# Performance work log

Measured on AMD Instinct MI355X. Metric: run time of the kernel, lower is better.

## Reference

```python
import jax, jax.numpy as jnp
import numpy as np

N_SENT, N_DOC, G = 100000, 10000, 32

def _seg_mean_right(x, src, dst, n_dst):
    # DGL GraphConv(norm='right'): sum incoming messages / in_degree (clamped to 1)
    m = jax.ops.segment_sum(x[src], dst, num_segments=n_dst)
    deg = jax.ops.segment_sum(jnp.ones_like(dst, dtype=x.dtype), dst, num_segments=n_dst)
    return m / jnp.maximum(deg, 1.0)[:, None]

def _rel_layer(xs, xd, coeff, basis, loop_w, bias,
               src_ss, dst_ss, src_sd, dst_sd, src_ds, dst_ds):
    # WeightBasis: per-relation weight = sum_b coeff[r,b] * basis[b]
    W = jnp.einsum('rb,bio->rio', coeff, basis)  # [3, in, out]
    # rel 0: sent->doc, rel 1: doc->sent, rel 2: sent->sent; HeteroGraphConv sums per dst ntype
    h_doc = _seg_mean_right(xs, src_sd, dst_sd, N_DOC) @ W[0]
    h_sent = (_seg_mean_right(xd, src_ds, dst_ds, N_SENT) @ W[1]
              + _seg_mean_right(xs, src_ss, dst_ss, N_SENT) @ W[2])
    h_sent = jax.nn.relu(h_sent + xs @ loop_w + bias)
    h_doc = jax.nn.relu(h_doc + xd @ loop_w + bias)
    return h_sent, h_doc

def setup_inputs() -> dict:
    key = jax.random.key(0)
    ks = jax.random.split(key, 20)
    d_in, d_h, d_o = 768, 256, 128
    inp = {
        'x_sent': jax.random.normal(ks[0], (N_SENT, d_in), jnp.float32),
        'x_doc': jax.random.normal(ks[1], (N_DOC, d_in), jnp.float32),
        'coeff1': jax.random.normal(ks[2], (3, 2), jnp.float32),
        'basis1': jax.random.normal(ks[3], (2, d_in, d_h), jnp.float32) * 0.02,
        'loop_w1': jax.random.normal(ks[4], (d_in, d_h), jnp.float32) * 0.02,
        'bias1': jnp.zeros((d_h,), jnp.float32),
        'coeff2': jax.random.normal(ks[5], (3, 2), jnp.float32),
        'basis2': jax.random.normal(ks[6], (2, d_h, d_o), jnp.float32) * 0.05,
        'loop_w2': jax.random.normal(ks[7], (d_h, d_o), jnp.float32) * 0.05,
        'bias2': jnp.zeros((d_o,), jnp.float32),
        'w_score': jax.random.normal(ks[8], (d_o, 1), jnp.float32) * 0.05,
        'b_score': jnp.zeros((1,), jnp.float32),
        'src_ss': jax.random.randint(ks[9], (400000,), 0, N_SENT, jnp.int32),
        'dst_ss': jax.random.randint(ks[10], (400000,), 0, N_SENT, jnp.int32),
        'src_sd': jax.random.randint(ks[11], (100000,), 0, N_SENT, jnp.int32),
        'dst_sd': jax.random.randint(ks[12], (100000,), 0, N_DOC, jnp.int32),
        'src_ds': jax.random.randint(ks[13], (100000,), 0, N_DOC, jnp.int32),
        'dst_ds': jax.random.randint(ks[14], (100000,), 0, N_SENT, jnp.int32),
        'gid_sent': jnp.sort(jax.random.randint(ks[15], (N_SENT,), 0, G, jnp.int32)),
        'gid_doc': jnp.sort(jax.random.randint(ks[16], (N_DOC,), 0, G, jnp.int32)),
        'num_graphs': G,
    }
    return inp

def reference(x_sent, x_doc, coeff1, basis1, loop_w1, bias1,
              coeff2, basis2, loop_w2, bias2, w_score, b_score,
              src_ss, dst_ss, src_sd, dst_sd, src_ds, dst_ds,
              gid_sent, gid_doc, num_graphs):
    h_s, h_d = _rel_layer(x_sent, x_doc, coeff1, basis1, loop_w1, bias1,
                          src_ss, dst_ss, src_sd, dst_sd, src_ds, dst_ds)
    h_s, h_d = _rel_layer(h_s, h_d, coeff2, basis2, loop_w2, bias2,
                          src_ss, dst_ss, src_sd, dst_sd, src_ds, dst_ds)
    # dgl.sum_nodes over batched graph, summed across ntypes
    readout = (jax.ops.segment_sum(h_s, gid_sent, num_segments=num_graphs)
               + jax.ops.segment_sum(h_d, gid_doc, num_segments=num_graphs))
    return readout @ w_score + b_score  # [G, 1]
```

## Files before the change

kernel.cpp:

```cpp
#include <hip/hip_runtime.h>

#define CDIV(a,b) (((a)+(b)-1)/(b))

typedef __attribute__((ext_vector_type(8))) short bf16x8;
typedef __attribute__((ext_vector_type(4))) float floatx4;

__device__ __forceinline__ ushort f2bf(float x) {
    unsigned u = __float_as_uint(x);
    return (ushort)((u + 0x7fffu + ((u >> 16) & 1u)) >> 16);
}
__device__ __forceinline__ float bflo(unsigned v) { return __uint_as_float(v << 16); }
__device__ __forceinline__ float bfhi(unsigned v) { return __uint_as_float(v & 0xffff0000u); }

__device__ __forceinline__ void load_lds16(const ushort* g, ushort* l) {
    __builtin_amdgcn_global_load_lds(
        (const __attribute__((address_space(1))) void*)g,
        (__attribute__((address_space(3))) void*)l, 16, 0, 0);
}


__global__ void zero_f4(float4* __restrict__ p, long long n4) {
    long long i = blockIdx.x * 256LL + threadIdx.x;
    if (i < n4) p[i] = make_float4(0.f, 0.f, 0.f, 0.f);
}

__global__ void cvt_bf16_k(const float4* __restrict__ in, uint4* __restrict__ out, long long n8) {
    long long i = blockIdx.x * 256LL + threadIdx.x;
    if (i >= n8) return;
    float4 a = in[2 * i], b = in[2 * i + 1];
    uint4 o;
    o.x = (unsigned)f2bf(a.x) | ((unsigned)f2bf(a.y) << 16);
    o.y = (unsigned)f2bf(a.z) | ((unsigned)f2bf(a.w) << 16);
    o.z = (unsigned)f2bf(b.x) | ((unsigned)f2bf(b.y) << 16);
    o.w = (unsigned)f2bf(b.z) | ((unsigned)f2bf(b.w) << 16);
    out[i] = o;
}

__global__ void fill_basis_T(ushort* __restrict__ out, int K, int col0,
                             const float* __restrict__ basis, long long KN,
                             const float* __restrict__ coeff, int r, int N, long long total) {
    long long i = blockIdx.x * 256LL + threadIdx.x;
    if (i >= total) return;
    int k = (int)(i % K), n = (int)(i / K);
    float c0 = coeff[2 * r], c1 = coeff[2 * r + 1];
    out[(size_t)(col0 + n) * K + k] = f2bf(c0 * basis[(size_t)k * N + n] + c1 * basis[KN + (size_t)k * N + n]);
}

__global__ void fill_copy_T(ushort* __restrict__ out, int K, int col0,
                            const float* __restrict__ src, int N, long long total) {
    long long i = blockIdx.x * 256LL + threadIdx.x;
    if (i >= total) return;
    int k = (int)(i % K), n = (int)(i / K);
    out[(size_t)(col0 + n) * K + k] = f2bf(src[(size_t)k * N + n]);
}


__global__ void accum_deg_i(const int* __restrict__ dst, int n, int slot, int* __restrict__ deg) {
    int i = blockIdx.x * 256 + threadIdx.x;
    if (i < n) atomicAdd(&deg[slot + dst[i]], 1);
}

__global__ void scan_p1(const int* __restrict__ deg, int n, int* __restrict__ bsum) {
    __shared__ int sd[256];
    int blk = blockIdx.x, tid = threadIdx.x;
    int i0 = blk * 1024 + tid * 4;
    int s = 0;
#pragma unroll
    for (int j = 0; j < 4; ++j) if (i0 + j < n) s += deg[i0 + j];
    sd[tid] = s; __syncthreads();
    for (int o = 128; o; o >>= 1) {
        if (tid < o) sd[tid] += sd[tid + o];
        __syncthreads();
    }
    if (tid == 0) bsum[blk] = sd[0];
}

__global__ void scan_p2(int* __restrict__ bsum, int nb, int* __restrict__ rowptr, int ntot, int etot) {
    __shared__ int sd[256];
    int tid = threadIdx.x;
    int v = (tid < nb) ? bsum[tid] : 0;
    sd[tid] = v; __syncthreads();
    for (int o = 1; o < 256; o <<= 1) {
        int t = (tid >= o) ? sd[tid - o] : 0;
        __syncthreads();
        sd[tid] += t;
        __syncthreads();
    }
    if (tid < nb) bsum[tid] = sd[tid] - v;
    if (tid == 0) rowptr[ntot] = etot;
}

__global__ void scan_p3(const int* __restrict__ deg, int n, const int* __restrict__ bsum,
                        int* __restrict__ rowptr) {
    __shared__ int sd[256];
    int blk = blockIdx.x, tid = threadIdx.x;
    int i0 = blk * 1024 + tid * 4;
    int v[4]; int s = 0;
#pragma unroll
    for (int j = 0; j < 4; ++j) { v[j] = (i0 + j < n) ? deg[i0 + j] : 0; s += v[j]; }
    sd[tid] = s; __syncthreads();
    for (int o = 1; o < 256; o <<= 1) {
        int t = (tid >= o) ? sd[tid - o] : 0;
        __syncthreads();
        sd[tid] += t;
        __syncthreads();
    }
    int excl = bsum[blk] + sd[tid] - s;
#pragma unroll
    for (int j = 0; j < 4; ++j) {
        if (i0 + j < n) rowptr[i0 + j] = excl;
        excl += v[j];
    }
}

__global__ void fill_csr(const int* __restrict__ src, const int* __restrict__ dst, int n, int slot,
                         const int* __restrict__ rowptr, int* __restrict__ fill, int* __restrict__ col) {
    int i = blockIdx.x * 256 + threadIdx.x;
    if (i >= n) return;
    int d = slot + dst[i];
    int p = rowptr[d] + atomicAdd(&fill[d], 1);
    col[p] = src[i];
}

__global__ __launch_bounds__(256) void gemm_bf16(
    const ushort* __restrict__ A, const ushort* __restrict__ Bt, ushort* __restrict__ C,
    int M, int K, int N) {
    __shared__ ushort As[128 * 32];
    __shared__ ushort Bs[128 * 32];
    const int tid = threadIdx.x;
    const int bn = blockIdx.x * 128;
    const long long bm = blockIdx.y * 128LL;
    const int lane = tid & 63, wave = tid >> 6;
    const int mo = (wave & 1) * 64, no = (wave >> 1) * 64;
    const int l15 = lane & 15, quad = lane >> 4;
    const int srow0 = wave * 16 + (lane >> 2);
    const int schunk = (lane & 3) * 8;
    floatx4 acc[4][4] = {};

    for (int k0 = 0; k0 < K; k0 += 32) {
#pragma unroll
        for (int t = 0; t < 2; ++t) {
            int row = t * 64 + srow0;
            long long ar = bm + row; if (ar >= M) ar = M - 1;
            load_lds16(A + ar * (size_t)K + k0 + schunk, As + t * 2048 + wave * 512);
            load_lds16(Bt + (size_t)(bn + row) * K + k0 + schunk, Bs + t * 2048 + wave * 512);
        }
        __syncthreads();
        bf16x8 af[4], bfr[4];
#pragma unroll
        for (int mt = 0; mt < 4; ++mt)
            af[mt] = *(const bf16x8*)(As + (mo + mt * 16 + l15) * 32 + quad * 8);
#pragma unroll
        for (int nt = 0; nt < 4; ++nt)
            bfr[nt] = *(const bf16x8*)(Bs + (no + nt * 16 + l15) * 32 + quad * 8);
#pragma unroll
        for (int mt = 0; mt < 4; ++mt)
#pragma unroll
            for (int nt = 0; nt < 4; ++nt)
                acc[mt][nt] = __builtin_amdgcn_mfma_f32_16x16x32_bf16(af[mt], bfr[nt], acc[mt][nt], 0, 0, 0);
        __syncthreads();
    }
#pragma unroll
    for (int mt = 0; mt < 4; ++mt)
#pragma unroll
        for (int i = 0; i < 4; ++i) {
            long long row = bm + mo + mt * 16 + quad * 4 + i;
            if (row < M) {
#pragma unroll
                for (int nt = 0; nt < 4; ++nt)
                    C[row * (size_t)N + bn + no + nt * 16 + l15] = f2bf(acc[mt][nt][i]);
            }
        }
}


__global__ __launch_bounds__(256) void fused_sent_l1(
    const ushort* __restrict__ ys, const ushort* __restrict__ yd,
    const int* __restrict__ rowptr, const int* __restrict__ col,
    const float* __restrict__ bias, ushort* __restrict__ hout, int NS) {
    int d = blockIdx.x * 4 + (threadIdx.x >> 6);
    if (d >= NS) return;
    int lane = threadIdx.x & 63;
    int cb = lane * 4;
    float a0 = 0, a1 = 0, a2 = 0, a3 = 0;
    int s0 = rowptr[d], s1 = rowptr[d + 1];
    for (int e = s0; e < s1; ++e) {
        int s = col[e];
        uint2 v = *(const uint2*)(ys + (size_t)s * 768 + 256 + cb);
        a0 += bflo(v.x); a1 += bfhi(v.x); a2 += bflo(v.y); a3 += bfhi(v.y);
    }
    float inv = 1.f / (float)max(s1 - s0, 1);
    float m0 = a0 * inv, m1 = a1 * inv, m2 = a2 * inv, m3 = a3 * inv;
    a0 = a1 = a2 = a3 = 0.f;
    int t0 = rowptr[NS + d], t1 = rowptr[NS + d + 1];
    for (int e = t0; e < t1; ++e) {
        int s = col[e];
        uint2 v = *(const uint2*)(yd + (size_t)s * 512 + cb);
        a0 += bflo(v.x); a1 += bfhi(v.x); a2 += bflo(v.y); a3 += bfhi(v.y);
    }
    inv = 1.f / (float)max(t1 - t0, 1);
    uint2 lv = *(const uint2*)(ys + (size_t)d * 768 + 512 + cb);
    float h0 = fmaxf(m0 + a0 * inv + bflo(lv.x) + bias[cb + 0], 0.f);
    float h1 = fmaxf(m1 + a1 * inv + bfhi(lv.x) + bias[cb + 1], 0.f);
    float h2 = fmaxf(m2 + a2 * inv + bflo(lv.y) + bias[cb + 2], 0.f);
    float h3 = fmaxf(m3 + a3 * inv + bfhi(lv.y) + bias[cb + 3], 0.f);
    uint2 o;
    o.x = (unsigned)f2bf(h0) | ((unsigned)f2bf(h1) << 16);
    o.y = (unsigned)f2bf(h2) | ((unsigned)f2bf(h3) << 16);
    *(uint2*)(hout + (size_t)d * 256 + cb) = o;
}

__global__ __launch_bounds__(256) void fused_doc_l1(
    const ushort* __restrict__ ys, const ushort* __restrict__ yd,
    const int* __restrict__ rowptr, const int* __restrict__ col,
    const float* __restrict__ bias, ushort* __restrict__ hout, int NS, int ND) {
    int d = blockIdx.x * 4 + (threadIdx.x >> 6);
    if (d >= ND) return;
    int lane = threadIdx.x & 63;
    int cb = lane * 4;
    float a0 = 0, a1 = 0, a2 = 0, a3 = 0;
    int s0 = rowptr[2 * NS + d], s1 = rowptr[2 * NS + d + 1];
    for (int e = s0; e < s1; ++e) {
        int s = col[e];
        uint2 v = *(const uint2*)(ys + (size_t)s * 768 + cb);
        a0 += bflo(v.x); a1 += bfhi(v.x); a2 += bflo(v.y); a3 += bfhi(v.y);
    }
    float inv = 1.f / (float)max(s1 - s0, 1);
    uint2 lv = *(const uint2*)(yd + (size_t)d * 512 + 256 + cb);
    float h0 = fmaxf(a0 * inv + bflo(lv.x) + bias[cb + 0], 0.f);
    float h1 = fmaxf(a1 * inv + bfhi(lv.x) + bias[cb + 1], 0.f);
    float h2 = fmaxf(a2 * inv + bflo(lv.y) + bias[cb + 2], 0.f);
    float h3 = fmaxf(a3 * inv + bfhi(lv.y) + bias[cb + 3], 0.f);
    uint2 o;
    o.x = (unsigned)f2bf(h0) | ((unsigned)f2bf(h1) << 16);
    o.y = (unsigned)f2bf(h2) | ((unsigned)f2bf(h3) << 16);
    *(uint2*)(hout + (size_t)d * 256 + cb) = o;
}

__global__ __launch_bounds__(256) void fused_sent_l2(
    const ushort* __restrict__ ys, const ushort* __restrict__ yd,
    const int* __restrict__ rowptr, const int* __restrict__ col,
    const float* __restrict__ bias, const float* __restrict__ w,
    const int* __restrict__ gid, float* __restrict__ out, int NS, int G) {
    __shared__ float part[4][32];
    const int tid = threadIdx.x;
    const int lane = tid & 63, wv = tid >> 6;
    const int cb = lane * 2;
    float racc = 0.f;
    const int nw = gridDim.x * 4;
    for (int d = blockIdx.x * 4 + wv; d < NS; d += nw) {
        float a0 = 0.f, a1 = 0.f;
        int s0 = rowptr[d], s1 = rowptr[d + 1];
        for (int e = s0; e < s1; ++e) {
            int s = col[e];
            unsigned v = *(const unsigned*)(ys + (size_t)s * 384 + 128 + cb);
            a0 += bflo(v); a1 += bfhi(v);
        }
        float inv = 1.f / (float)max(s1 - s0, 1);
        float m0 = a0 * inv, m1 = a1 * inv;
        a0 = 0.f; a1 = 0.f;
        int t0 = rowptr[NS + d], t1 = rowptr[NS + d + 1];
        for (int e = t0; e < t1; ++e) {
            int s = col[e];
            unsigned v = *(const unsigned*)(yd + (size_t)s * 256 + cb);
            a0 += bflo(v); a1 += bfhi(v);
        }
        inv = 1.f / (float)max(t1 - t0, 1);
        unsigned lv = *(const unsigned*)(ys + (size_t)d * 384 + 256 + cb);
        float h0 = fmaxf(m0 + a0 * inv + bflo(lv) + bias[cb + 0], 0.f);
        float h1 = fmaxf(m1 + a1 * inv + bfhi(lv) + bias[cb + 1], 0.f);
        float sc = h0 * w[cb] + h1 * w[cb + 1];
#pragma unroll
        for (int o = 32; o; o >>= 1) sc += __shfl_down(sc, o);
        sc = __shfl(sc, 0);
        if (lane == gid[d]) racc += sc;
    }
    if (lane < 32) part[wv][lane] = racc;
    __syncthreads();
    if (tid < G) atomicAdd(&out[tid], part[0][tid] + part[1][tid] + part[2][tid] + part[3][tid]);
}

__global__ __launch_bounds__(256) void fused_doc_l2(
    const ushort* __restrict__ ys, const ushort* __restrict__ yd,
    const int* __restrict__ rowptr, const int* __restrict__ col,
    const float* __restrict__ bias, const float* __restrict__ w,
    const int* __restrict__ gid, float* __restrict__ out, int NS, int ND, int G) {
    __shared__ float part[4][32];
    const int tid = threadIdx.x;
    const int lane = tid & 63, wv = tid >> 6;
    const int cb = lane * 2;
    float racc = 0.f;
    const int nw = gridDim.x * 4;
    for (int d = blockIdx.x * 4 + wv; d < ND; d += nw) {
        float a0 = 0.f, a1 = 0.f;
        int s0 = rowptr[2 * NS + d], s1 = rowptr[2 * NS + d + 1];
        for (int e = s0; e < s1; ++e) {
            int s = col[e];
            unsigned v = *(const unsigned*)(ys + (size_t)s * 384 + cb);
            a0 += bflo(v); a1 += bfhi(v);
        }
        float inv = 1.f / (float)max(s1 - s0, 1);
        unsigned lv = *(const unsigned*)(yd + (size_t)d * 256 + 128 + cb);
        float h0 = fmaxf(a0 * inv + bflo(lv) + bias[cb + 0], 0.f);
        float h1 = fmaxf(a1 * inv + bfhi(lv) + bias[cb + 1], 0.f);
        float sc = h0 * w[cb] + h1 * w[cb + 1];
#pragma unroll
        for (int o = 32; o; o >>= 1) sc += __shfl_down(sc, o);
        sc = __shfl(sc, 0);
        if (lane == gid[d]) racc += sc;
    }
    if (lane < 32) part[wv][lane] = racc;
    __syncthreads();
    if (tid < G) atomicAdd(&out[tid], part[0][tid] + part[1][tid] + part[2][tid] + part[3][tid]);
}

__global__ void init_out(float* __restrict__ out, const float* __restrict__ b, int G) {
    int i = threadIdx.x;
    if (i < G) out[i] = b[0];
}


extern "C" void kernel_launch(void* const* d_in, const int* in_sizes, int n_in,
                              void* d_out, int out_size, void* d_ws, size_t ws_size,
                              hipStream_t stream) {
    const float* x_sent = (const float*)d_in[0];
    const float* x_doc  = (const float*)d_in[1];
    const float* coeff1 = (const float*)d_in[2];
    const float* basis1 = (const float*)d_in[3];
    const float* loopw1 = (const float*)d_in[4];
    const float* bias1  = (const float*)d_in[5];
    const float* coeff2 = (const float*)d_in[6];
    const float* basis2 = (const float*)d_in[7];
    const float* loopw2 = (const float*)d_in[8];
    const float* bias2  = (const float*)d_in[9];
    const float* wscore = (const float*)d_in[10];
    const float* bscore = (const float*)d_in[11];
    const int* src_ss = (const int*)d_in[12];
    const int* dst_ss = (const int*)d_in[13];
    const int* src_sd = (const int*)d_in[14];
    const int* dst_sd = (const int*)d_in[15];
    const int* src_ds = (const int*)d_in[16];
    const int* dst_ds = (const int*)d_in[17];
    const int* gid_sent = (const int*)d_in[18];
    const int* gid_doc  = (const int*)d_in[19];

    const int DIN = 768, DH = 256, DOo = 128;
    const int NS = in_sizes[0] / DIN;
    const int ND = in_sizes[1] / DIN;
    const int E_SS = in_sizes[12], E_SD = in_sizes[14], E_DS = in_sizes[16];
    const int NTOT = NS + NS + ND;
    const int ETOT = E_SS + E_DS + E_SD;
    const int G = out_size;
    float* out = (float*)d_out;

    char* base = (char*)d_ws;
    size_t off = 0;
    auto alloc = [&](size_t bytes) -> char* {
        char* p = base + off;
        off = (off + bytes + 255) & ~(size_t)255;
        return p;
    };
    ushort* B1sT = (ushort*)alloc((size_t)768 * 768 * 2);
    ushort* B1dT = (ushort*)alloc((size_t)512 * 768 * 2);
    ushort* B2sT = (ushort*)alloc((size_t)384 * 256 * 2);
    ushort* B2dT = (ushort*)alloc((size_t)256 * 256 * 2);
    ushort* xs_bf = (ushort*)alloc((size_t)NS * 768 * 2);
    ushort* xd_bf = (ushort*)alloc((size_t)ND * 768 * 2);
    ushort* ys1 = (ushort*)alloc((size_t)NS * 768 * 2);
    ushort* yd1 = (ushort*)alloc((size_t)ND * 512 * 2);
    ushort* h1s = (ushort*)alloc((size_t)NS * 256 * 2);
    ushort* h1d = (ushort*)alloc((size_t)ND * 256 * 2);
    int* deg  = (int*)alloc((size_t)2 * NTOT * 4);
    int* fill = deg + NTOT;
    int* rowptr = (int*)alloc((size_t)(NTOT + 1) * 4);
    int* bsum = (int*)alloc(256 * 4);
    int* colall = (int*)alloc((size_t)ETOT * 4);
    ushort* ys2 = xs_bf;
    ushort* yd2 = xs_bf + (size_t)NS * 384;

    long long t1 = (long long)768 * DH, t2 = (long long)256 * DOo;
    long long KN1 = t1, KN2 = t2;
    int bt1 = (int)CDIV(t1, 256), bt2 = (int)CDIV(t2, 256);
    fill_basis_T<<<bt1, 256, 0, stream>>>(B1sT, 768, 0,       basis1, KN1, coeff1, 0, DH, t1);
    fill_basis_T<<<bt1, 256, 0, stream>>>(B1sT, 768, DH,      basis1, KN1, coeff1, 2, DH, t1);
    fill_copy_T <<<bt1, 256, 0, stream>>>(B1sT, 768, 2 * DH,  loopw1, DH, t1);
    fill_basis_T<<<bt1, 256, 0, stream>>>(B1dT, 768, 0,       basis1, KN1, coeff1, 1, DH, t1);
    fill_copy_T <<<bt1, 256, 0, stream>>>(B1dT, 768, DH,      loopw1, DH, t1);
    fill_basis_T<<<bt2, 256, 0, stream>>>(B2sT, 256, 0,        basis2, KN2, coeff2, 0, DOo, t2);
    fill_basis_T<<<bt2, 256, 0, stream>>>(B2sT, 256, DOo,      basis2, KN2, coeff2, 2, DOo, t2);
    fill_copy_T <<<bt2, 256, 0, stream>>>(B2sT, 256, 2 * DOo,  loopw2, DOo, t2);
    fill_basis_T<<<bt2, 256, 0, stream>>>(B2dT, 256, 0,        basis2, KN2, coeff2, 1, DOo, t2);
    fill_copy_T <<<bt2, 256, 0, stream>>>(B2dT, 256, DOo,      loopw2, DOo, t2);

    cvt_bf16_k<<<(int)CDIV((long long)NS * 768 / 8, 256), 256, 0, stream>>>(
        (const float4*)x_sent, (uint4*)xs_bf, (long long)NS * 768 / 8);
    cvt_bf16_k<<<(int)CDIV((long long)ND * 768 / 8, 256), 256, 0, stream>>>(
        (const float4*)x_doc, (uint4*)xd_bf, (long long)ND * 768 / 8);

    zero_f4<<<(int)CDIV(2 * NTOT / 4, 256), 256, 0, stream>>>((float4*)deg, 2 * NTOT / 4);
    accum_deg_i<<<CDIV(E_SS, 256), 256, 0, stream>>>(dst_ss, E_SS, 0,      deg);
    accum_deg_i<<<CDIV(E_DS, 256), 256, 0, stream>>>(dst_ds, E_DS, NS,     deg);
    accum_deg_i<<<CDIV(E_SD, 256), 256, 0, stream>>>(dst_sd, E_SD, 2 * NS, deg);
    int nb = CDIV(NTOT, 1024);
    scan_p1<<<nb, 256, 0, stream>>>(deg, NTOT, bsum);
    scan_p2<<<1, 256, 0, stream>>>(bsum, nb, rowptr, NTOT, ETOT);
    scan_p3<<<nb, 256, 0, stream>>>(deg, NTOT, bsum, rowptr);
    fill_csr<<<CDIV(E_SS, 256), 256, 0, stream>>>(src_ss, dst_ss, E_SS, 0,      rowptr, fill, colall);
    fill_csr<<<CDIV(E_DS, 256), 256, 0, stream>>>(src_ds, dst_ds, E_DS, NS,     rowptr, fill, colall);
    fill_csr<<<CDIV(E_SD, 256), 256, 0, stream>>>(src_sd, dst_sd, E_SD, 2 * NS, rowptr, fill, colall);

    {
        dim3 g(768 / 128, CDIV(NS, 128));
        gemm_bf16<<<g, 256, 0, stream>>>(xs_bf, B1sT, ys1, NS, 768, 768);
    }
    {
        dim3 g(512 / 128, CDIV(ND, 128));
        gemm_bf16<<<g, 256, 0, stream>>>(xd_bf, B1dT, yd1, ND, 768, 512);
    }
    fused_sent_l1<<<CDIV(NS, 4), 256, 0, stream>>>(ys1, yd1, rowptr, colall, bias1, h1s, NS);
    fused_doc_l1 <<<CDIV(ND, 4), 256, 0, stream>>>(ys1, yd1, rowptr, colall, bias1, h1d, NS, ND);

    {
        dim3 g(384 / 128, CDIV(NS, 128));
        gemm_bf16<<<g, 256, 0, stream>>>(h1s, B2sT, ys2, NS, 256, 384);
    }
    {
        dim3 g(256 / 128, CDIV(ND, 128));
        gemm_bf16<<<g, 256, 0, stream>>>(h1d, B2dT, yd2, ND, 256, 256);
    }
    init_out<<<1, 64, 0, stream>>>(out, bscore, G);
    fused_sent_l2<<<1024, 256, 0, stream>>>(ys2, yd2, rowptr, colall, bias2, wscore, gid_sent, out, NS, G);
    fused_doc_l2 <<<256, 256, 0, stream>>>(ys2, yd2, rowptr, colall, bias2, wscore, gid_doc, out, NS, ND, G);
}
```

Before: 1.169 ms.

## Merge per-relation launches into combined kernels and unroll gather loops

Merges the weight-fill, bf16-conversion, degree-count, CSR-fill and gather kernels into single launches that cover all relations and node types through index-range dispatch. The gather loops are unrolled by four so several neighbor-row loads are in flight at once, and bias and score weights are hoisted into registers. The first sentence GEMM is split into two launches over halves of the rows. These changes cut launch count and raise memory-level parallelism in the gathers, at the cost of more branching inside each kernel.

```diff
diff --git a/kernel.cpp b/kernel.cpp
--- a/kernel.cpp
+++ b/kernel.cpp
@@ -24,40 +24,50 @@
     if (i < n4) p[i] = make_float4(0.f, 0.f, 0.f, 0.f);
 }
 
-__global__ void cvt_bf16_k(const float4* __restrict__ in, uint4* __restrict__ out, long long n8) {
+__global__ void cvt_all(const float4* __restrict__ xs, const float4* __restrict__ xd,
+                        uint4* __restrict__ os, uint4* __restrict__ od,
+                        long long n8s, long long n8d) {
     long long i = blockIdx.x * 256LL + threadIdx.x;
-    if (i >= n8) return;
-    float4 a = in[2 * i], b = in[2 * i + 1];
+    const float4* in; uint4* out; long long j;
+    if (i < n8s) { in = xs; out = os; j = i; }
+    else if (i < n8s + n8d) { in = xd; out = od; j = i - n8s; }
+    else return;
+    float4 a = in[2 * j], b = in[2 * j + 1];
     uint4 o;
     o.x = (unsigned)f2bf(a.x) | ((unsigned)f2bf(a.y) << 16);
     o.y = (unsigned)f2bf(a.z) | ((unsigned)f2bf(a.w) << 16);
     o.z = (unsigned)f2bf(b.x) | ((unsigned)f2bf(b.y) << 16);
     o.w = (unsigned)f2bf(b.z) | ((unsigned)f2bf(b.w) << 16);
-    out[i] = o;
-}
-
-__global__ void fill_basis_T(ushort* __restrict__ out, int K, int col0,
-                             const float* __restrict__ basis, long long KN,
-                             const float* __restrict__ coeff, int r, int N, long long total) {
+    out[j] = o;
+}
+
+__global__ void fill_w5(ushort* __restrict__ BsT, ushort* __restrict__ BdT,
+                        const float* __restrict__ basis, const float* __restrict__ loopw,
+                        const float* __restrict__ coeff, int K, int N, long long KN) {
     long long i = blockIdx.x * 256LL + threadIdx.x;
-    if (i >= total) return;
+    if (i >= KN) return;
     int k = (int)(i % K), n = (int)(i / K);
-    float c0 = coeff[2 * r], c1 = coeff[2 * r + 1];
-    out[(size_t)(col0 + n) * K + k] = f2bf(c0 * basis[(size_t)k * N + n] + c1 * basis[KN + (size_t)k * N + n]);
-}
-
-__global__ void fill_copy_T(ushort* __restrict__ out, int K, int col0,
-                            const float* __restrict__ src, int N, long long total) {
-    long long i = blockIdx.x * 256LL + threadIdx.x;
-    if (i >= total) return;
-    int k = (int)(i % K), n = (int)(i / K);
-    out[(size_t)(col0 + n) * K + k] = f2bf(src[(size_t)k * N + n]);
-}
-
-
-__global__ void accum_deg_i(const int* __restrict__ dst, int n, int slot, int* __restrict__ deg) {
+    int sec = blockIdx.y;
+    float val;
+    if (sec == 2 || sec == 4) {
+        val = loopw[(size_t)k * N + n];
+    } else {
+        int r = (sec == 0) ? 0 : (sec == 1) ? 2 : 1;
+        val = coeff[2 * r] * basis[(size_t)k * N + n] + coeff[2 * r + 1] * basis[KN + (size_t)k * N + n];
+    }
+    ushort* dst = (sec < 3) ? BsT : BdT;
+    int col0 = (sec == 0) ? 0 : (sec == 1) ? N : (sec == 2) ? 2 * N : (sec == 3) ? 0 : N;
+    dst[(size_t)(col0 + n) * K + k] = f2bf(val);
+}
+
+
+__global__ void accum_deg_all(const int* __restrict__ dss, const int* __restrict__ dds,
+                              const int* __restrict__ dsd, int nss, int nds, int nsd,
+                              int NS, int* __restrict__ deg) {
     int i = blockIdx.x * 256 + threadIdx.x;
-    if (i < n) atomicAdd(&deg[slot + dst[i]], 1);
+    if (i < nss) atomicAdd(&deg[dss[i]], 1);
+    else if (i < nss + nds) atomicAdd(&deg[NS + dds[i - nss]], 1);
+    else if (i < nss + nds + nsd) atomicAdd(&deg[2 * NS + dsd[i - nss - nds]], 1);
 }
 
 __global__ void scan_p1(const int* __restrict__ deg, int n, int* __restrict__ bsum) {
@@ -113,13 +123,20 @@
     }
 }
 
-__global__ void fill_csr(const int* __restrict__ src, const int* __restrict__ dst, int n, int slot,
-                         const int* __restrict__ rowptr, int* __restrict__ fill, int* __restrict__ col) {
+__global__ void fill_csr_all(const int* __restrict__ sss, const int* __restrict__ dss,
+                             const int* __restrict__ sds, const int* __restrict__ dds,
+                             const int* __restrict__ ssd, const int* __restrict__ dsd,
+                             int nss, int nds, int nsd, int NS,
+                             const int* __restrict__ rowptr, int* __restrict__ fill,
+                             int* __restrict__ col) {
     int i = blockIdx.x * 256 + threadIdx.x;
-    if (i >= n) return;
-    int d = slot + dst[i];
+    int d, s;
+    if (i < nss) { d = dss[i]; s = sss[i]; }
+    else if (i < nss + nds) { int j = i - nss; d = NS + dds[j]; s = sds[j]; }
+    else if (i < nss + nds + nsd) { int j = i - nss - nds; d = 2 * NS + dsd[j]; s = ssd[j]; }
+    else return;
     int p = rowptr[d] + atomicAdd(&fill[d], 1);
-    col[p] = src[i];
+    col[p] = s;
 }
 
 __global__ __launch_bounds__(256) void gemm_bf16(
@@ -174,140 +191,166 @@
 }
 
 
-__global__ __launch_bounds__(256) void fused_sent_l1(
+__global__ __launch_bounds__(256) void gather_l1(
     const ushort* __restrict__ ys, const ushort* __restrict__ yd,
     const int* __restrict__ rowptr, const int* __restrict__ col,
-    const float* __restrict__ bias, ushort* __restrict__ hout, int NS) {
+    const float* __restrict__ bias, ushort* __restrict__ h1s, ushort* __restrict__ h1d,
+    int NS, int ND) {
     int d = blockIdx.x * 4 + (threadIdx.x >> 6);
-    if (d >= NS) return;
     int lane = threadIdx.x & 63;
     int cb = lane * 4;
-    float a0 = 0, a1 = 0, a2 = 0, a3 = 0;
-    int s0 = rowptr[d], s1 = rowptr[d + 1];
-    for (int e = s0; e < s1; ++e) {
-        int s = col[e];
-        uint2 v = *(const uint2*)(ys + (size_t)s * 768 + 256 + cb);
-        a0 += bflo(v.x); a1 += bfhi(v.x); a2 += bflo(v.y); a3 += bfhi(v.y);
-    }
-    float inv = 1.f / (float)max(s1 - s0, 1);
-    float m0 = a0 * inv, m1 = a1 * inv, m2 = a2 * inv, m3 = a3 * inv;
-    a0 = a1 = a2 = a3 = 0.f;
-    int t0 = rowptr[NS + d], t1 = rowptr[NS + d + 1];
-    for (int e = t0; e < t1; ++e) {
-        int s = col[e];
-        uint2 v = *(const uint2*)(yd + (size_t)s * 512 + cb);
-        a0 += bflo(v.x); a1 += bfhi(v.x); a2 += bflo(v.y); a3 += bfhi(v.y);
-    }
-    inv = 1.f / (float)max(t1 - t0, 1);
-    uint2 lv = *(const uint2*)(ys + (size_t)d * 768 + 512 + cb);
-    float h0 = fmaxf(m0 + a0 * inv + bflo(lv.x) + bias[cb + 0], 0.f);
-    float h1 = fmaxf(m1 + a1 * inv + bfhi(lv.x) + bias[cb + 1], 0.f);
-    float h2 = fmaxf(m2 + a2 * inv + bflo(lv.y) + bias[cb + 2], 0.f);
-    float h3 = fmaxf(m3 + a3 * inv + bfhi(lv.y) + bias[cb + 3], 0.f);
-    uint2 o;
-    o.x = (unsigned)f2bf(h0) | ((unsigned)f2bf(h1) << 16);
-    o.y = (unsigned)f2bf(h2) | ((unsigned)f2bf(h3) << 16);
-    *(uint2*)(hout + (size_t)d * 256 + cb) = o;
-}
-
-__global__ __launch_bounds__(256) void fused_doc_l1(
-    const ushort* __restrict__ ys, const ushort* __restrict__ yd,
-    const int* __restrict__ rowptr, const int* __restrict__ col,
-    const float* __restrict__ bias, ushort* __restrict__ hout, int NS, int ND) {
-    int d = blockIdx.x * 4 + (threadIdx.x >> 6);
-    if (d >= ND) return;
-    int lane = threadIdx.x & 63;
-    int cb = lane * 4;
-    float a0 = 0, a1 = 0, a2 = 0, a3 = 0;
-    int s0 = rowptr[2 * NS + d], s1 = rowptr[2 * NS + d + 1];
-    for (int e = s0; e < s1; ++e) {
-        int s = col[e];
-        uint2 v = *(const uint2*)(ys + (size_t)s * 768 + cb);
-        a0 += bflo(v.x); a1 += bfhi(v.x); a2 += bflo(v.y); a3 += bfhi(v.y);
-    }
-    float inv = 1.f / (float)max(s1 - s0, 1);
-    uint2 lv = *(const uint2*)(yd + (size_t)d * 512 + 256 + cb);
-    float h0 = fmaxf(a0 * inv + bflo(lv.x) + bias[cb + 0], 0.f);
-    float h1 = fmaxf(a1 * inv + bfhi(lv.x) + bias[cb + 1], 0.f);
-    float h2 = fmaxf(a2 * inv + bflo(lv.y) + bias[cb + 2], 0.f);
-    float h3 = fmaxf(a3 * inv + bfhi(lv.y) + bias[cb + 3], 0.f);
-    uint2 o;
-    o.x = (unsigned)f2bf(h0) | ((unsigned)f2bf(h1) << 16);
-    o.y = (unsigned)f2bf(h2) | ((unsigned)f2bf(h3) << 16);
-    *(uint2*)(hout + (size_t)d * 256 + cb) = o;
-}
-
-__global__ __launch_bounds__(256) void fused_sent_l2(
+    float b0 = bias[cb], b1 = bias[cb + 1], b2 = bias[cb + 2], b3 = bias[cb + 3];
+    if (d < NS) {
+        float a0 = 0, a1 = 0, a2 = 0, a3 = 0;
+        int s0 = rowptr[d], s1 = rowptr[d + 1];
+        int e = s0;
+        for (; e + 4 <= s1; e += 4) {
+            int sA = col[e], sB = col[e + 1], sC = col[e + 2], sD = col[e + 3];
+            uint2 vA = *(const uint2*)(ys + (size_t)sA * 768 + 256 + cb);
+            uint2 vB = *(const uint2*)(ys + (size_t)sB * 768 + 256 + cb);
+            uint2 vC = *(const uint2*)(ys + (size_t)sC * 768 + 256 + cb);
+            uint2 vD = *(const uint2*)(ys + (size_t)sD * 768 + 256 + cb);
+            a0 += bflo(vA.x) + bflo(vB.x) + bflo(vC.x) + bflo(vD.x);
+            a1 += bfhi(vA.x) + bfhi(vB.x) + bfhi(vC.x) + bfhi(vD.x);
+            a2 += bflo(vA.y) + bflo(vB.y) + bflo(vC.y) + bflo(vD.y);
+            a3 += bfhi(vA.y) + bfhi(vB.y) + bfhi(vC.y) + bfhi(vD.y);
+        }
+        for (; e < s1; ++e) {
+            int s = col[e];
+            uint2 v = *(const uint2*)(ys + (size_t)s * 768 + 256 + cb);
+            a0 += bflo(v.x); a1 += bfhi(v.x); a2 += bflo(v.y); a3 += bfhi(v.y);
+        }
+        float inv = 1.f / (float)max(s1 - s0, 1);
+        float m0 = a0 * inv, m1 = a1 * inv, m2 = a2 * inv, m3 = a3 * inv;
+        a0 = a1 = a2 = a3 = 0.f;
+        int t0 = rowptr[NS + d], t1 = rowptr[NS + d + 1];
+        for (e = t0; e < t1; ++e) {
+            int s = col[e];
+            uint2 v = *(const uint2*)(yd + (size_t)s * 512 + cb);
+            a0 += bflo(v.x); a1 += bfhi(v.x); a2 += bflo(v.y); a3 += bfhi(v.y);
+        }
+        inv = 1.f / (float)max(t1 - t0, 1);
+        uint2 lv = *(const uint2*)(ys + (size_t)d * 768 + 512 + cb);
+        float h0 = fmaxf(m0 + a0 * inv + bflo(lv.x) + b0, 0.f);
+        float h1 = fmaxf(m1 + a1 * inv + bfhi(lv.x) + b1, 0.f);
+        float h2 = fmaxf(m2 + a2 * inv + bflo(lv.y) + b2, 0.f);
+        float h3 = fmaxf(m3 + a3 * inv + bfhi(lv.y) + b3, 0.f);
+        uint2 o;
+        o.x = (unsigned)f2bf(h0) | ((unsigned)f2bf(h1) << 16);
+        o.y = (unsigned)f2bf(h2) | ((unsigned)f2bf(h3) << 16);
+        *(uint2*)(h1s + (size_t)d * 256 + cb) = o;
+    } else if (d < NS + ND) {
+        int dd = d - NS;
+        float a0 = 0, a1 = 0, a2 = 0, a3 = 0;
+        int s0 = rowptr[2 * NS + dd], s1 = rowptr[2 * NS + dd + 1];
+        int e = s0;
+        for (; e + 4 <= s1; e += 4) {
+            int sA = col[e], sB = col[e + 1], sC = col[e + 2], sD = col[e + 3];
+            uint2 vA = *(const uint2*)(ys + (size_t)sA * 768 + cb);
+            uint2 vB = *(const uint2*)(ys + (size_t)sB * 768 + cb);
+            uint2 vC = *(const uint2*)(ys + (size_t)sC * 768 + cb);
+            uint2 vD = *(const uint2*)(ys + (size_t)sD * 768 + cb);
+            a0 += bflo(vA.x) + bflo(vB.x) + bflo(vC.x) + bflo(vD.x);
+            a1 += bfhi(vA.x) + bfhi(vB.x) + bfhi(vC.x) + bfhi(vD.x);
+            a2 += bflo(vA.y) + bflo(vB.y) + bflo(vC.y) + bflo(vD.y);
+            a3 += bfhi(vA.y) + bfhi(vB.y) + bfhi(vC.y) + bfhi(vD.y);
+        }
+        for (; e < s1; ++e) {
+            int s = col[e];
+            uint2 v = *(const uint2*)(ys + (size_t)s * 768 + cb);
+            a0 += bflo(v.x); a1 += bfhi(v.x); a2 += bflo(v.y); a3 += bfhi(v.y);
+        }
+        float inv = 1.f / (float)max(s1 - s0, 1);
+        uint2 lv = *(const uint2*)(yd + (size_t)dd * 512 + 256 + cb);
+        float h0 = fmaxf(a0 * inv + bflo(lv.x) + b0, 0.f);
+        float h1 = fmaxf(a1 * inv + bfhi(lv.x) + b1, 0.f);
+        float h2 = fmaxf(a2 * inv + bflo(lv.y) + b2, 0.f);
+        float h3 = fmaxf(a3 * inv + bfhi(lv.y) + b3, 0.f);
+        uint2 o;
+        o.x = (unsigned)f2bf(h0) | ((unsigned)f2bf(h1) << 16);
+        o.y = (unsigned)f2bf(h2) | ((unsigned)f2bf(h3) << 16);
+        *(uint2*)(h1d + (size_t)dd * 256 + cb) = o;
+    }
+}
+
+__global__ __launch_bounds__(256) void gather_l2(
     const ushort* __restrict__ ys, const ushort* __restrict__ yd,
     const int* __restrict__ rowptr, const int* __restrict__ col,
     const float* __restrict__ bias, const float* __restrict__ w,
-    const int* __restrict__ gid, float* __restrict__ out, int NS, int G) {
+    const int* __restrict__ gid_s, const int* __restrict__ gid_d,
+    float* __restrict__ out, int NS, int ND, int G) {
     __shared__ float part[4][32];
     const int tid = threadIdx.x;
     const int lane = tid & 63, wv = tid >> 6;
     const int cb = lane * 2;
+    const float w0 = w[cb], w1 = w[cb + 1];
+    const float b0 = bias[cb], b1 = bias[cb + 1];
     float racc = 0.f;
     const int nw = gridDim.x * 4;
-    for (int d = blockIdx.x * 4 + wv; d < NS; d += nw) {
-        float a0 = 0.f, a1 = 0.f;
-        int s0 = rowptr[d], s1 = rowptr[d + 1];
-        for (int e = s0; e < s1; ++e) {
-            int s = col[e];
-            unsigned v = *(const unsigned*)(ys + (size_t)s * 384 + 128 + cb);
-            a0 += bflo(v); a1 += bfhi(v);
-        }
-        float inv = 1.f / (float)max(s1 - s0, 1);
-        float m0 = a0 * inv, m1 = a1 * inv;
-        a0 = 0.f; a1 = 0.f;
-        int t0 = rowptr[NS + d], t1 = rowptr[NS + d + 1];
-        for (int e = t0; e < t1; ++e) {
-            int s = col[e];
-            unsigned v = *(const unsigned*)(yd + (size_t)s * 256 + cb);
-            a0 += bflo(v); a1 += bfhi(v);
-        }
-        inv = 1.f / (float)max(t1 - t0, 1);
-        unsigned lv = *(const unsigned*)(ys + (size_t)d * 384 + 256 + cb);
-        float h0 = fmaxf(m0 + a0 * inv + bflo(lv) + bias[cb + 0], 0.f);
-        float h1 = fmaxf(m1 + a1 * inv + bfhi(lv) + bias[cb + 1], 0.f);
-        float sc = h0 * w[cb] + h1 * w[cb + 1];
+    for (int d = blockIdx.x * 4 + wv; d < NS + ND; d += nw) {
+        float h0, h1; int g;
+        if (d < NS) {
+            float a0 = 0.f, a1 = 0.f;
+            int s0 = rowptr[d], s1 = rowptr[d + 1];
+            int e = s0;
+            for (; e + 4 <= s1; e += 4) {
+                int sA = col[e], sB = col[e + 1], sC = col[e + 2], sD = col[e + 3];
+                unsigned vA = *(const unsigned*)(ys + (size_t)sA * 384 + 128 + cb);
+                unsigned vB = *(const unsigned*)(ys + (size_t)sB * 384 + 128 + cb);
+                unsigned vC = *(const unsigned*)(ys + (size_t)sC * 384 + 128 + cb);
+                unsigned vD = *(const unsigned*)(ys + (size_t)sD * 384 + 128 + cb);
+                a0 += bflo(vA) + bflo(vB) + bflo(vC) + bflo(vD);
+                a1 += bfhi(vA) + bfhi(vB) + bfhi(vC) + bfhi(vD);
+            }
+            for (; e < s1; ++e) {
+                int s = col[e];
+                unsigned v = *(const unsigned*)(ys + (size_t)s * 384 + 128 + cb);
+                a0 += bflo(v); a1 += bfhi(v);
+            }
+            float inv = 1.f / (float)max(s1 - s0, 1);
+            float m0 = a0 * inv, m1 = a1 * inv;
+            a0 = 0.f; a1 = 0.f;
+            int t0 = rowptr[NS + d], t1 = rowptr[NS + d + 1];
+            for (e = t0; e < t1; ++e) {
+                int s = col[e];
+                unsigned v = *(const unsigned*)(yd + (size_t)s * 256 + cb);
+                a0 += bflo(v); a1 += bfhi(v);
+            }
+            inv = 1.f / (float)max(t1 - t0, 1);
+            unsigned lv = *(const unsigned*)(ys + (size_t)d * 384 + 256 + cb);
+            h0 = fmaxf(m0 + a0 * inv + bflo(lv) + b0, 0.f);
+            h1 = fmaxf(m1 + a1 * inv + bfhi(lv) + b1, 0.f);
+            g = gid_s[d];
+        } else {
+            int dd = d - NS;
+            float a0 = 0.f, a1 = 0.f;
+            int s0 = rowptr[2 * NS + dd], s1 = rowptr[2 * NS + dd + 1];
+            int e = s0;
+            for (; e + 4 <= s1; e += 4) {
+                int sA = col[e], sB = col[e + 1], sC = col[e + 2], sD = col[e + 3];
+                unsigned vA = *(const unsigned*)(ys + (size_t)sA * 384 + cb);
+                unsigned vB = *(const unsigned*)(ys + (size_t)sB * 384 + cb);
+                unsigned vC = *(const unsigned*)(ys + (size_t)sC * 384 + cb);
+                unsigned vD = *(const unsigned*)(ys + (size_t)sD * 384 + cb);
+                a0 += bflo(vA) + bflo(vB) + bflo(vC) + bflo(vD);
+                a1 += bfhi(vA) + bfhi(vB) + bfhi(vC) + bfhi(vD);
+            }
+            for (; e < s1; ++e) {
+                int s = col[e];
+                unsigned v = *(const unsigned*)(ys + (size_t)s * 384 + cb);
+                a0 += bflo(v); a1 += bfhi(v);
+            }
+            float inv = 1.f / (float)max(s1 - s0, 1);
+            unsigned lv = *(const unsigned*)(yd + (size_t)dd * 256 + 128 + cb);
+            h0 = fmaxf(a0 * inv + bflo(lv) + b0, 0.f);
+            h1 = fmaxf(a1 * inv + bfhi(lv) + b1, 0.f);
+            g = gid_d[dd];
+        }
+        float sc = h0 * w0 + h1 * w1;
 #pragma unroll
         for (int o = 32; o; o >>= 1) sc += __shfl_down(sc, o);
         sc = __shfl(sc, 0);
-        if (lane == gid[d]) racc += sc;
-    }
-    if (lane < 32) part[wv][lane] = racc;
-    __syncthreads();
-    if (tid < G) atomicAdd(&out[tid], part[0][tid] + part[1][tid] + part[2][tid] + part[3][tid]);
-}
-
-__global__ __launch_bounds__(256) void fused_doc_l2(
-    const ushort* __restrict__ ys, const ushort* __restrict__ yd,
-    const int* __restrict__ rowptr, const int* __restrict__ col,
-    const float* __restrict__ bias, const float* __restrict__ w,
-    const int* __restrict__ gid, float* __restrict__ out, int NS, int ND, int G) {
-    __shared__ float part[4][32];
-    const int tid = threadIdx.x;
-    const int lane = tid & 63, wv = tid >> 6;
-    const int cb = lane * 2;
-    float racc = 0.f;
-    const int nw = gridDim.x * 4;
-    for (int d = blockIdx.x * 4 + wv; d < ND; d += nw) {
-        float a0 = 0.f, a1 = 0.f;
-        int s0 = rowptr[2 * NS + d], s1 = rowptr[2 * NS + d + 1];
-        for (int e = s0; e < s1; ++e) {
-            int s = col[e];
-            unsigned v = *(const unsigned*)(ys + (size_t)s * 384 + cb);
-            a0 += bflo(v); a1 += bfhi(v);
-        }
-        float inv = 1.f / (float)max(s1 - s0, 1);
-        unsigned lv = *(const unsigned*)(yd + (size_t)d * 256 + 128 + cb);
-        float h0 = fmaxf(a0 * inv + bflo(lv) + bias[cb + 0], 0.f);
-        float h1 = fmaxf(a1 * inv + bfhi(lv) + bias[cb + 1], 0.f);
-        float sc = h0 * w[cb] + h1 * w[cb + 1];
-#pragma unroll
-        for (int o = 32; o; o >>= 1) sc += __shfl_down(sc, o);
-        sc = __shfl(sc, 0);
-        if (lane == gid[d]) racc += sc;
+        if (lane == g) racc += sc;
     }
     if (lane < 32) part[wv][lane] = racc;
     __syncthreads();
@@ -379,56 +422,37 @@
     ushort* yd2 = xs_bf + (size_t)NS * 384;
 
     long long t1 = (long long)768 * DH, t2 = (long long)256 * DOo;
-    long long KN1 = t1, KN2 = t2;
-    int bt1 = (int)CDIV(t1, 256), bt2 = (int)CDIV(t2, 256);
-    fill_basis_T<<<bt1, 256, 0, stream>>>(B1sT, 768, 0,       basis1, KN1, coeff1, 0, DH, t1);
-    fill_basis_T<<<bt1, 256, 0, stream>>>(B1sT, 768, DH,      basis1, KN1, coeff1, 2, DH, t1);
-    fill_copy_T <<<bt1, 256, 0, stream>>>(B1sT, 768, 2 * DH,  loopw1, DH, t1);
-    fill_basis_T<<<bt1, 256, 0, stream>>>(B1dT, 768, 0,       basis1, KN1, coeff1, 1, DH, t1);
-    fill_copy_T <<<bt1, 256, 0, stream>>>(B1dT, 768, DH,      loopw1, DH, t1);
-    fill_basis_T<<<bt2, 256, 0, stream>>>(B2sT, 256, 0,        basis2, KN2, coeff2, 0, DOo, t2);
-    fill_basis_T<<<bt2, 256, 0, stream>>>(B2sT, 256, DOo,      basis2, KN2, coeff2, 2, DOo, t2);
-    fill_copy_T <<<bt2, 256, 0, stream>>>(B2sT, 256, 2 * DOo,  loopw2, DOo, t2);
-    fill_basis_T<<<bt2, 256, 0, stream>>>(B2dT, 256, 0,        basis2, KN2, coeff2, 1, DOo, t2);
-    fill_copy_T <<<bt2, 256, 0, stream>>>(B2dT, 256, DOo,      loopw2, DOo, t2);
-
-    cvt_bf16_k<<<(int)CDIV((long long)NS * 768 / 8, 256), 256, 0, stream>>>(
-        (const float4*)x_sent, (uint4*)xs_bf, (long long)NS * 768 / 8);
-    cvt_bf16_k<<<(int)CDIV((long long)ND * 768 / 8, 256), 256, 0, stream>>>(
-        (const float4*)x_doc, (uint4*)xd_bf, (long long)ND * 768 / 8);
+    fill_w5<<<dim3((unsigned)CDIV(t1, 256), 5), 256, 0, stream>>>(B1sT, B1dT, basis1, loopw1, coeff1, 768, DH, t1);
+    fill_w5<<<dim3((unsigned)CDIV(t2, 256), 5), 256, 0, stream>>>(B2sT, B2dT, basis2, loopw2, coeff2, 256, DOo, t2);
+
+    long long n8s = (long long)NS * 96, n8d = (long long)ND * 96;
+    cvt_all<<<(int)CDIV(n8s + n8d, 256), 256, 0, stream>>>(
+        (const float4*)x_sent, (const float4*)x_doc, (uint4*)xs_bf, (uint4*)xd_bf, n8s, n8d);
 
     zero_f4<<<(int)CDIV(2 * NTOT / 4, 256), 256, 0, stream>>>((float4*)deg, 2 * NTOT / 4);
-    accum_deg_i<<<CDIV(E_SS, 256), 256, 0, stream>>>(dst_ss, E_SS, 0,      deg);
-    accum_deg_i<<<CDIV(E_DS, 256), 256, 0, stream>>>(dst_ds, E_DS, NS,     deg);
-    accum_deg_i<<<CDIV(E_SD, 256), 256, 0, stream>>>(dst_sd, E_SD, 2 * NS, deg);
+    accum_deg_all<<<CDIV(ETOT, 256), 256, 0, stream>>>(dst_ss, dst_ds, dst_sd, E_SS, E_DS, E_SD, NS, deg);
     int nb = CDIV(NTOT, 1024);
     scan_p1<<<nb, 256, 0, stream>>>(deg, NTOT, bsum);
     scan_p2<<<1, 256, 0, stream>>>(bsum, nb, rowptr, NTOT, ETOT);
     scan_p3<<<nb, 256, 0, stream>>>(deg, NTOT, bsum, rowptr);
-    fill_csr<<<CDIV(E_SS, 256), 256, 0, stream>>>(src_ss, dst_ss, E_SS, 0,      rowptr, fill, colall);
-    fill_csr<<<CDIV(E_DS, 256), 256, 0, stream>>>(src_ds, dst_ds, E_DS, NS,     rowptr, fill, colall);
-    fill_csr<<<CDIV(E_SD, 256), 256, 0, stream>>>(src_sd, dst_sd, E_SD, 2 * NS, rowptr, fill, colall);
+    fill_csr_all<<<CDIV(ETOT, 256), 256, 0, stream>>>(src_ss, dst_ss, src_ds, dst_ds, src_sd, dst_sd,
+                                                      E_SS, E_DS, E_SD, NS, rowptr, fill, colall);
 
     {
-        dim3 g(768 / 128, CDIV(NS, 128));
-        gemm_bf16<<<g, 256, 0, stream>>>(xs_bf, B1sT, ys1, NS, 768, 768);
-    }
-    {
-        dim3 g(512 / 128, CDIV(ND, 128));
-        gemm_bf16<<<g, 256, 0, stream>>>(xd_bf, B1dT, yd1, ND, 768, 512);
-    }
-    fused_sent_l1<<<CDIV(NS, 4), 256, 0, stream>>>(ys1, yd1, rowptr, colall, bias1, h1s, NS);
-    fused_doc_l1 <<<CDIV(ND, 4), 256, 0, stream>>>(ys1, yd1, rowptr, colall, bias1, h1d, NS, ND);
-
-    {
-        dim3 g(384 / 128, CDIV(NS, 128));
-        gemm_bf16<<<g, 256, 0, stream>>>(h1s, B2sT, ys2, NS, 256, 384);
-    }
-    {
-        dim3 g(256 / 128, CDIV(ND, 128));
-        gemm_bf16<<<g, 256, 0, stream>>>(h1d, B2dT, yd2, ND, 256, 256);
-    }
+        int mb = CDIV(NS, 128), mb0 = mb / 2;
+        int M0 = mb0 * 128;
+        gemm_bf16<<<dim3(6, mb0), 256, 0, stream>>>(xs_bf, B1sT, ys1, M0, 768, 768);
+        gemm_bf16<<<dim3(6, mb - mb0), 256, 0, stream>>>(
+            xs_bf + (size_t)M0 * 768, B1sT, ys1 + (size_t)M0 * 768, NS - M0, 768, 768);
+    }
+    gemm_bf16<<<dim3(4, CDIV(ND, 128)), 256, 0, stream>>>(xd_bf, B1dT, yd1, ND, 768, 512);
+
+    gather_l1<<<CDIV(NS + ND, 4), 256, 0, stream>>>(ys1, yd1, rowptr, colall, bias1, h1s, h1d, NS, ND);
+
+    gemm_bf16<<<dim3(3, CDIV(NS, 128)), 256, 0, stream>>>(h1s, B2sT, ys2, NS, 256, 384);
+    gemm_bf16<<<dim3(2, CDIV(ND, 128)), 256, 0, stream>>>(h1d, B2dT, yd2, ND, 256, 256);
+
     init_out<<<1, 64, 0, stream>>>(out, bscore, G);
-    fused_sent_l2<<<1024, 256, 0, stream>>>(ys2, yd2, rowptr, colall, bias2, wscore, gid_sent, out, NS, G);
-    fused_doc_l2 <<<256, 256, 0, stream>>>(ys2, yd2, rowptr, colall, bias2, wscore, gid_doc, out, NS, ND, G);
-}
+    gather_l2<<<1100, 256, 0, stream>>>(ys2, yd2, rowptr, colall, bias2, wscore,
+                                        gid_sent, gid_doc, out, NS, ND, G);
+}
```

Result: faster. 1.051 ms (-10.1%).
